# Optimization experiments

Hardware: AMD Instinct MI355X
Metric: run time of the kernel (lower is better)

## Reference

```python
import jax, jax.numpy as jnp
import numpy as np

WS = 8          # window size
NUM_HEADS = 12


def setup_inputs() -> dict:
    key = jax.random.key(0)
    k1, k2, k3 = jax.random.split(key, 3)
    B, N, C = 16, 4096, 384
    x = jax.random.normal(k1, (B, N, C), dtype=jnp.float32)
    # torch Linear weights stored as [in, out] so forward is x @ W
    qkv_w = jax.random.normal(k2, (C, 3 * C), dtype=jnp.float32) * (C ** -0.5)
    proj_w = jax.random.normal(k3, (C, C), dtype=jnp.float32) * (C ** -0.5)
    proj_b = jnp.zeros((C,), dtype=jnp.float32)
    return {"x": x, "qkv_w": qkv_w, "proj_w": proj_w, "proj_b": proj_b}


def reference(x, qkv_w, proj_w, proj_b):
    B, N, C = x.shape
    H = W = int(np.sqrt(N))
    hg, wg = H // WS, W // WS
    G = hg * wg
    nh = NUM_HEADS
    hd = C // nh
    scale = hd ** -0.5

    # window partition: [B, N, C] -> [B, hg, wg, ws, ws, C]
    xw = x.reshape(B, hg, WS, wg, WS, C).transpose(0, 1, 3, 2, 4, 5)
    xw = xw.reshape(B, G, WS * WS, C)

    # qkv projection -> [3, B, G, nh, ws*ws, hd]
    qkv = (xw @ qkv_w).reshape(B, G, WS * WS, 3, nh, hd)
    qkv = qkv.transpose(3, 0, 1, 4, 2, 5)
    q, k, v = qkv[0], qkv[1], qkv[2]

    attn = jnp.einsum('bgnqd,bgnkd->bgnqk', q, k) * scale
    attn = jax.nn.softmax(attn, axis=-1)
    out = jnp.einsum('bgnqk,bgnkd->bgnqd', attn, v)

    # merge heads and reverse window partition
    out = out.transpose(0, 1, 3, 2, 4).reshape(B, hg, wg, WS, WS, C)
    out = out.transpose(0, 1, 3, 2, 4, 5).reshape(B, N, C)

    return out @ proj_w + proj_b
```

## Files before the change

kernel.cpp:

```cpp
#include <hip/hip_runtime.h>
#include <stdint.h>

typedef unsigned short ushort_t;
typedef __bf16 bf16x8 __attribute__((ext_vector_type(8)));
typedef float floatx4 __attribute__((ext_vector_type(4)));
typedef float floatx16 __attribute__((ext_vector_type(16)));
typedef unsigned short ushort8 __attribute__((ext_vector_type(8)));

__device__ __forceinline__ ushort_t f2b(float f) {
  union { float f; unsigned u; } v; v.f = f;
  unsigned r = v.u + 0x7fffu + ((v.u >> 16) & 1u);
  return (ushort_t)(r >> 16);
}
__device__ __forceinline__ ushort_t b2u(float f) {
  union { __bf16 b; ushort_t u; } v; v.b = (__bf16)f; return v.u;
}
__device__ __forceinline__ bf16x8 cvt8(const float* p) {
  floatx4 f0 = *(const floatx4*)p;
  floatx4 f1 = *(const floatx4*)(p + 4);
  union { bf16x8 v; __bf16 e[8]; } u;
#pragma unroll
  for (int j = 0; j < 4; ++j) u.e[j] = (__bf16)f0[j];
#pragma unroll
  for (int j = 0; j < 4; ++j) u.e[4 + j] = (__bf16)f1[j];
  return u.v;
}

__device__ __forceinline__ unsigned cvtpk(float a, float b) {
  unsigned r;
  asm("v_cvt_pk_bf16_f32 %0, %1, %2" : "=v"(r) : "v"(a), "v"(b));
  return r;
}
__device__ __forceinline__ void plswap(unsigned& x, unsigned& y) {
  asm("v_permlane32_swap_b32 %0, %1" : "+v"(x), "+v"(y));
}

__device__ __forceinline__ void async16(const ushort_t* g, ushort_t* l) {
  __builtin_amdgcn_global_load_lds(
      (const __attribute__((address_space(1))) void*)g,
      (__attribute__((address_space(3))) void*)l, 16, 0, 0);
}

__global__ __launch_bounds__(256) void cvt_x(const float* __restrict__ src,
                                             ushort_t* __restrict__ dst, int n8) {
  int i = blockIdx.x * 256 + threadIdx.x;
  if (i < n8) *(bf16x8*)&dst[(size_t)i * 8] = cvt8(src + (size_t)i * 8);
}

__global__ void transpose_k(const float* __restrict__ src,
                            ushort_t* __restrict__ dst, int R, int Cc) {
  int idx = blockIdx.x * 256 + threadIdx.x;
  if (idx < R * Cc) {
    int r = idx / Cc, c = idx % Cc;
    dst[(size_t)c * R + r] = f2b(src[idx]);
  }
}

template <int C_F32>
__global__ __launch_bounds__(256) void gemm_bt(
    const ushort_t* __restrict__ A, int lda,
    const ushort_t* __restrict__ Bt,
    const float* __restrict__ bias, void* __restrict__ C_,
    int M, int N, int K) {
  __shared__ __align__(16) ushort_t As[128 * 64];
  __shared__ __align__(16) ushort_t Bs[128 * 64];
  const int t = threadIdx.x;
  const int nwg = gridDim.x;
  const int per = nwg >> 3;
  const int swz = (blockIdx.x & 7) * per + (blockIdx.x >> 3);
  const int ntn = N >> 7;
  const int m0 = (swz / ntn) << 7;
  const int n0 = (swz % ntn) << 7;
  const int w = t >> 6, lane = t & 63;
  const int wy = (w >> 1) << 6;
  const int wx = (w & 1) << 6;
  const int l15 = lane & 15;
  const int quad = lane >> 4;
  const int quad4 = quad << 2;
  floatx4 acc[4][4] = {};
  const int srow = t >> 3;
  const int sc = (((t & 7) ^ (srow & 7)) << 3);
  const ushort_t* gA = A + (size_t)(m0 + srow) * lda + sc;
  const ushort_t* gB = Bt + (size_t)(n0 + srow) * K + sc;
  for (int k0 = 0; k0 < K; k0 += 64) {
    __syncthreads();
#pragma unroll
    for (int r4 = 0; r4 < 4; ++r4) {
      async16(gA + (size_t)r4 * 32 * lda + k0, &As[r4 * 2048 + t * 8]);
      async16(gB + (size_t)r4 * 32 * K + k0, &Bs[r4 * 2048 + t * 8]);
    }
    __syncthreads();
#pragma unroll
    for (int kk = 0; kk < 2; ++kk) {
      bf16x8 af[4], bfr[4];
#pragma unroll
      for (int i = 0; i < 4; ++i) {
        int row = wy + i * 16 + l15;
        af[i] = *(const bf16x8*)&As[row * 64 + ((((kk << 2) | quad) ^ (row & 7)) << 3)];
      }
#pragma unroll
      for (int j = 0; j < 4; ++j) {
        int row = wx + j * 16 + l15;
        bfr[j] = *(const bf16x8*)&Bs[row * 64 + ((((kk << 2) | quad) ^ (row & 7)) << 3)];
      }
#pragma unroll
      for (int i = 0; i < 4; ++i)
#pragma unroll
        for (int j = 0; j < 4; ++j)
          acc[i][j] = __builtin_amdgcn_mfma_f32_16x16x32_bf16(
              af[i], bfr[j], acc[i][j], 0, 0, 0);
    }
  }
  float bv[4] = {0.f, 0.f, 0.f, 0.f};
  if (bias != nullptr) {
#pragma unroll
    for (int j = 0; j < 4; ++j) bv[j] = bias[n0 + wx + j * 16 + l15];
  }
#pragma unroll
  for (int i = 0; i < 4; ++i) {
#pragma unroll
    for (int r = 0; r < 4; ++r) {
      size_t row = (size_t)(m0 + wy + i * 16 + quad4 + r);
      if (C_F32) {
        float* cp = (float*)C_ + row * N + (n0 + wx + l15);
#pragma unroll
        for (int j = 0; j < 4; ++j) cp[j * 16] = acc[i][j][r] + bv[j];
      } else {
        ushort_t* cp = (ushort_t*)C_ + row * N + (n0 + wx + l15);
#pragma unroll
        for (int j = 0; j < 4; ++j) cp[j * 16] = f2b(acc[i][j][r] + bv[j]);
      }
    }
  }
}

__global__ __launch_bounds__(256, 2) void attn_proj(
    const ushort_t* __restrict__ QKV, const ushort_t* __restrict__ Bt,
    const float* __restrict__ bias, float* __restrict__ out) {
  __shared__ __align__(16) ushort_t Vt[4][32 * 72];
  __shared__ __align__(16) ushort_t Ao[64 * 384];
  const int blk = blockIdx.x;
  const int b = blk >> 6, g = blk & 63;
  const int gy = g >> 3, gx = g & 7;
  const int t = threadIdx.x, w = t >> 6, lane = t & 63;
  const int l31 = lane & 31, bh = lane >> 5;
  const int l15 = lane & 15, quad = lane >> 4, quad4 = quad << 2;
  const size_t bbase = (size_t)b * 4096 + (size_t)(gy * 8) * 64 + gx * 8;
  const float scale = 0.17677669529663687f;

  for (int hi = 0; hi < 3; ++hi) {
    const int h = w * 3 + hi;
    const size_t hq = (size_t)h * 32;

    {
      size_t row = bbase + (size_t)(lane >> 3) * 64 + (lane & 7);
      const ushort_t* vp = QKV + row * 1152 + 768 + hq;
#pragma unroll
      for (int i = 0; i < 4; ++i) {
        ushort8 vv = *(const ushort8*)(vp + i * 8);
#pragma unroll
        for (int j = 0; j < 8; ++j) Vt[w][(i * 8 + j) * 72 + lane] = vv[j];
      }
    }

    bf16x8 qf[2][2];
#pragma unroll
    for (int qt = 0; qt < 2; ++qt) {
      int tok = qt * 32 + l31;
      size_t row = bbase + (size_t)(tok >> 3) * 64 + (tok & 7);
#pragma unroll
      for (int dc = 0; dc < 2; ++dc)
        qf[qt][dc] = *(const bf16x8*)(QKV + row * 1152 + hq + dc * 16 + bh * 8);
    }

    floatx16 st[2][2] = {};
#pragma unroll
    for (int kt = 0; kt < 2; ++kt) {
      bf16x8 kf[2];
      int tok = kt * 32 + l31;
      size_t row = bbase + (size_t)(tok >> 3) * 64 + (tok & 7);
#pragma unroll
      for (int dc = 0; dc < 2; ++dc)
        kf[dc] = *(const bf16x8*)(QKV + row * 1152 + 384 + hq + dc * 16 + bh * 8);
#pragma unroll
      for (int qt = 0; qt < 2; ++qt)
#pragma unroll
        for (int dc = 0; dc < 2; ++dc)
          st[kt][qt] = __builtin_amdgcn_mfma_f32_32x32x16_bf16(
              kf[dc], qf[qt][dc], st[kt][qt], 0, 0, 0);
    }

    float rs[2] = {0.f, 0.f};
#pragma unroll
    for (int kt = 0; kt < 2; ++kt)
#pragma unroll
      for (int qt = 0; qt < 2; ++qt)
#pragma unroll
        for (int r = 0; r < 16; ++r) {
          float e = __expf(st[kt][qt][r] * scale);
          st[kt][qt][r] = e;
          rs[qt] += e;
        }
#pragma unroll
    for (int qt = 0; qt < 2; ++qt) rs[qt] += __shfl_xor(rs[qt], 32);
    float inv[2] = {1.0f / rs[0], 1.0f / rs[1]};

    floatx16 o[2] = {};
#pragma unroll
    for (int s = 0; s < 4; ++s) {
      const int kt = s >> 1, r1x = (s & 1) << 1;
      bf16x8 vf = *(const bf16x8*)&Vt[w][l31 * 72 + s * 16 + bh * 8];
#pragma unroll
      for (int qt = 0; qt < 2; ++qt) {
        float iv = inv[qt];
        unsigned x0 = cvtpk(st[kt][qt][4 * r1x + 0] * iv, st[kt][qt][4 * r1x + 1] * iv);
        unsigned x1 = cvtpk(st[kt][qt][4 * r1x + 2] * iv, st[kt][qt][4 * r1x + 3] * iv);
        unsigned y0 = cvtpk(st[kt][qt][4 * r1x + 4] * iv, st[kt][qt][4 * r1x + 5] * iv);
        unsigned y1 = cvtpk(st[kt][qt][4 * r1x + 6] * iv, st[kt][qt][4 * r1x + 7] * iv);
        plswap(x0, y0);
        plswap(x1, y1);
        union { unsigned d[4]; bf16x8 v; } pa;
        pa.d[0] = x0; pa.d[1] = x1; pa.d[2] = y0; pa.d[3] = y1;
        o[qt] = __builtin_amdgcn_mfma_f32_32x32x16_bf16(pa.v, vf, o[qt], 0, 0, 0);
      }
    }

    const int base64 = (h >> 1) << 6;
    const int cbase = ((h & 1) << 2) | (l31 >> 3);
    const int e7 = l31 & 7;
#pragma unroll
    for (int qt = 0; qt < 2; ++qt)
#pragma unroll
      for (int r = 0; r < 16; ++r) {
        int tok = qt * 32 + (r & 3) + 8 * (r >> 2) + 4 * bh;
        int c = cbase ^ (tok & 7);
        Ao[tok * 384 + base64 + (c << 3) + e7] = b2u(o[qt][r]);
      }
  }

  __syncthreads();

  floatx4 acc[4][6] = {};
  for (int ks = 0; ks < 12; ++ks) {
    bf16x8 af[4];
#pragma unroll
    for (int i = 0; i < 4; ++i) {
      int row = i * 16 + l15;
      int c = (((ks & 1) << 2) | quad) ^ (row & 7);
      af[i] = *(const bf16x8*)&Ao[row * 384 + ((ks >> 1) << 6) + (c << 3)];
    }
    bf16x8 bfr[6];
#pragma unroll
    for (int j = 0; j < 6; ++j) {
      int n = w * 96 + j * 16 + l15;
      bfr[j] = *(const bf16x8*)&Bt[(size_t)n * 384 + ks * 32 + (quad << 3)];
    }
#pragma unroll
    for (int i = 0; i < 4; ++i)
#pragma unroll
      for (int j = 0; j < 6; ++j)
        acc[i][j] = __builtin_amdgcn_mfma_f32_16x16x32_bf16(
            af[i], bfr[j], acc[i][j], 0, 0, 0);
  }

  float bv[6];
#pragma unroll
  for (int j = 0; j < 6; ++j) bv[j] = bias[w * 96 + j * 16 + l15];
#pragma unroll
  for (int i = 0; i < 4; ++i) {
#pragma unroll
    for (int r = 0; r < 4; ++r) {
      int tok = i * 16 + quad4 + r;
      size_t grow = bbase + (size_t)(tok >> 3) * 64 + (tok & 7);
      float* cp = out + grow * 384 + w * 96 + l15;
#pragma unroll
      for (int j = 0; j < 6; ++j) cp[j * 16] = acc[i][j][r] + bv[j];
    }
  }
}

extern "C" void kernel_launch(void* const* d_in, const int* in_sizes, int n_in,
                              void* d_out, int out_size, void* d_ws, size_t ws_size,
                              hipStream_t stream) {
  const float* x      = (const float*)d_in[0];
  const float* qkv_w  = (const float*)d_in[1];
  const float* proj_w = (const float*)d_in[2];
  const float* proj_b = (const float*)d_in[3];
  float* out = (float*)d_out;

  const int M = 16 * 4096;
  const size_t need =
      ((size_t)M * 1152 + (size_t)M * 384 + 1152 * 384 + 384 * 384) * 2;
  if (ws_size < need) return;

  ushort_t* qkv    = (ushort_t*)d_ws;
  ushort_t* xb     = qkv + (size_t)M * 1152;
  ushort_t* qkvwT  = xb + (size_t)M * 384;
  ushort_t* projwT = qkvwT + (size_t)1152 * 384;

  cvt_x<<<(M * 384 / 8 + 255) / 256, 256, 0, stream>>>(x, xb, M * 384 / 8);
  transpose_k<<<(384 * 1152 + 255) / 256, 256, 0, stream>>>(qkv_w, qkvwT, 384, 1152);
  transpose_k<<<(384 * 384 + 255) / 256, 256, 0, stream>>>(proj_w, projwT, 384, 384);

  gemm_bt<0><<<(M / 128) * (1152 / 128), 256, 0, stream>>>(
      xb, 384, qkvwT, nullptr, qkv, M, 1152, 384);

  attn_proj<<<16 * 64, 256, 0, stream>>>(qkv, projwT, proj_b, out);
}
```

Baseline: 329.6 us.

## Fuse fp32-to-bf16 input conversion into QKV GEMM and drop V LDS transpose

Removes the separate cvt_x kernel and bf16 copy of x; the QKV GEMM now reads fp32 x directly and converts it to bf16 while staging A tiles into LDS. In the attention kernel the V tile is no longer transposed through LDS but gathered with strided scalar global loads, K loads are hoisted ahead of the MFMAs, and occupancy is raised to 3 blocks per SM. This cuts one full read-write pass over x and LDS traffic, but the A loads become synchronous (no global_load_lds), each GEMM tile re-reads fp32 x nine times across N tiles, and the V gathers are uncoalesced 2-byte loads.

```diff
diff --git a/kernel.cpp b/kernel.cpp
--- a/kernel.cpp
+++ b/kernel.cpp
@@ -39,12 +39,6 @@
   __builtin_amdgcn_global_load_lds(
       (const __attribute__((address_space(1))) void*)g,
       (__attribute__((address_space(3))) void*)l, 16, 0, 0);
-}
-
-__global__ __launch_bounds__(256) void cvt_x(const float* __restrict__ src,
-                                             ushort_t* __restrict__ dst, int n8) {
-  int i = blockIdx.x * 256 + threadIdx.x;
-  if (i < n8) *(bf16x8*)&dst[(size_t)i * 8] = cvt8(src + (size_t)i * 8);
 }
 
 __global__ void transpose_k(const float* __restrict__ src,
@@ -56,12 +50,10 @@
   }
 }
 
-template <int C_F32>
-__global__ __launch_bounds__(256) void gemm_bt(
-    const ushort_t* __restrict__ A, int lda,
+__global__ __launch_bounds__(256) void gemm_qkv(
+    const float* __restrict__ A,
     const ushort_t* __restrict__ Bt,
-    const float* __restrict__ bias, void* __restrict__ C_,
-    int M, int N, int K) {
+    ushort_t* __restrict__ C, int M, int N, int K) {
   __shared__ __align__(16) ushort_t As[128 * 64];
   __shared__ __align__(16) ushort_t Bs[128 * 64];
   const int t = threadIdx.x;
@@ -80,14 +72,15 @@
   floatx4 acc[4][4] = {};
   const int srow = t >> 3;
   const int sc = (((t & 7) ^ (srow & 7)) << 3);
-  const ushort_t* gA = A + (size_t)(m0 + srow) * lda + sc;
+  const float* gA = A + (size_t)(m0 + srow) * K + sc;
   const ushort_t* gB = Bt + (size_t)(n0 + srow) * K + sc;
   for (int k0 = 0; k0 < K; k0 += 64) {
     __syncthreads();
 #pragma unroll
     for (int r4 = 0; r4 < 4; ++r4) {
-      async16(gA + (size_t)r4 * 32 * lda + k0, &As[r4 * 2048 + t * 8]);
       async16(gB + (size_t)r4 * 32 * K + k0, &Bs[r4 * 2048 + t * 8]);
+      bf16x8 av = cvt8(gA + (size_t)r4 * 32 * K + k0);
+      *(bf16x8*)&As[r4 * 2048 + t * 8] = av;
     }
     __syncthreads();
 #pragma unroll
@@ -111,33 +104,21 @@
               af[i], bfr[j], acc[i][j], 0, 0, 0);
     }
   }
-  float bv[4] = {0.f, 0.f, 0.f, 0.f};
-  if (bias != nullptr) {
-#pragma unroll
-    for (int j = 0; j < 4; ++j) bv[j] = bias[n0 + wx + j * 16 + l15];
-  }
 #pragma unroll
   for (int i = 0; i < 4; ++i) {
 #pragma unroll
     for (int r = 0; r < 4; ++r) {
       size_t row = (size_t)(m0 + wy + i * 16 + quad4 + r);
-      if (C_F32) {
-        float* cp = (float*)C_ + row * N + (n0 + wx + l15);
-#pragma unroll
-        for (int j = 0; j < 4; ++j) cp[j * 16] = acc[i][j][r] + bv[j];
-      } else {
-        ushort_t* cp = (ushort_t*)C_ + row * N + (n0 + wx + l15);
-#pragma unroll
-        for (int j = 0; j < 4; ++j) cp[j * 16] = f2b(acc[i][j][r] + bv[j]);
-      }
-    }
-  }
-}
-
-__global__ __launch_bounds__(256, 2) void attn_proj(
+      ushort_t* cp = C + row * N + (n0 + wx + l15);
+#pragma unroll
+      for (int j = 0; j < 4; ++j) cp[j * 16] = f2b(acc[i][j][r]);
+    }
+  }
+}
+
+__global__ __launch_bounds__(256, 3) void attn_proj(
     const ushort_t* __restrict__ QKV, const ushort_t* __restrict__ Bt,
     const float* __restrict__ bias, float* __restrict__ out) {
-  __shared__ __align__(16) ushort_t Vt[4][32 * 72];
   __shared__ __align__(16) ushort_t Ao[64 * 384];
   const int blk = blockIdx.x;
   const int b = blk >> 6, g = blk & 63;
@@ -152,17 +133,6 @@
     const int h = w * 3 + hi;
     const size_t hq = (size_t)h * 32;
 
-    {
-      size_t row = bbase + (size_t)(lane >> 3) * 64 + (lane & 7);
-      const ushort_t* vp = QKV + row * 1152 + 768 + hq;
-#pragma unroll
-      for (int i = 0; i < 4; ++i) {
-        ushort8 vv = *(const ushort8*)(vp + i * 8);
-#pragma unroll
-        for (int j = 0; j < 8; ++j) Vt[w][(i * 8 + j) * 72 + lane] = vv[j];
-      }
-    }
-
     bf16x8 qf[2][2];
 #pragma unroll
     for (int qt = 0; qt < 2; ++qt) {
@@ -172,23 +142,35 @@
       for (int dc = 0; dc < 2; ++dc)
         qf[qt][dc] = *(const bf16x8*)(QKV + row * 1152 + hq + dc * 16 + bh * 8);
     }
-
-    floatx16 st[2][2] = {};
+    bf16x8 kf[2][2];
 #pragma unroll
     for (int kt = 0; kt < 2; ++kt) {
-      bf16x8 kf[2];
       int tok = kt * 32 + l31;
       size_t row = bbase + (size_t)(tok >> 3) * 64 + (tok & 7);
 #pragma unroll
       for (int dc = 0; dc < 2; ++dc)
-        kf[dc] = *(const bf16x8*)(QKV + row * 1152 + 384 + hq + dc * 16 + bh * 8);
+        kf[kt][dc] = *(const bf16x8*)(QKV + row * 1152 + 384 + hq + dc * 16 + bh * 8);
+    }
+    bf16x8 vf[4];
+#pragma unroll
+    for (int s = 0; s < 4; ++s) {
+      const ushort_t* vbase =
+          QKV + (bbase + (size_t)(2 * s + bh) * 64) * 1152 + 768 + hq + l31;
+      union { ushort_t e[8]; bf16x8 v; } vu;
+#pragma unroll
+      for (int j = 0; j < 8; ++j) vu.e[j] = vbase[(size_t)j * 1152];
+      vf[s] = vu.v;
+    }
+
+    floatx16 st[2][2] = {};
+#pragma unroll
+    for (int kt = 0; kt < 2; ++kt)
 #pragma unroll
       for (int qt = 0; qt < 2; ++qt)
 #pragma unroll
         for (int dc = 0; dc < 2; ++dc)
           st[kt][qt] = __builtin_amdgcn_mfma_f32_32x32x16_bf16(
-              kf[dc], qf[qt][dc], st[kt][qt], 0, 0, 0);
-    }
+              kf[kt][dc], qf[qt][dc], st[kt][qt], 0, 0, 0);
 
     float rs[2] = {0.f, 0.f};
 #pragma unroll
@@ -209,7 +191,6 @@
 #pragma unroll
     for (int s = 0; s < 4; ++s) {
       const int kt = s >> 1, r1x = (s & 1) << 1;
-      bf16x8 vf = *(const bf16x8*)&Vt[w][l31 * 72 + s * 16 + bh * 8];
 #pragma unroll
       for (int qt = 0; qt < 2; ++qt) {
         float iv = inv[qt];
@@ -221,7 +202,7 @@
         plswap(x1, y1);
         union { unsigned d[4]; bf16x8 v; } pa;
         pa.d[0] = x0; pa.d[1] = x1; pa.d[2] = y0; pa.d[3] = y1;
-        o[qt] = __builtin_amdgcn_mfma_f32_32x32x16_bf16(pa.v, vf, o[qt], 0, 0, 0);
+        o[qt] = __builtin_amdgcn_mfma_f32_32x32x16_bf16(pa.v, vf[s], o[qt], 0, 0, 0);
       }
     }
 
@@ -290,20 +271,18 @@
 
   const int M = 16 * 4096;
   const size_t need =
-      ((size_t)M * 1152 + (size_t)M * 384 + 1152 * 384 + 384 * 384) * 2;
+      ((size_t)M * 1152 + 1152 * 384 + 384 * 384) * 2;
   if (ws_size < need) return;
 
   ushort_t* qkv    = (ushort_t*)d_ws;
-  ushort_t* xb     = qkv + (size_t)M * 1152;
-  ushort_t* qkvwT  = xb + (size_t)M * 384;
+  ushort_t* qkvwT  = qkv + (size_t)M * 1152;
   ushort_t* projwT = qkvwT + (size_t)1152 * 384;
 
-  cvt_x<<<(M * 384 / 8 + 255) / 256, 256, 0, stream>>>(x, xb, M * 384 / 8);
   transpose_k<<<(384 * 1152 + 255) / 256, 256, 0, stream>>>(qkv_w, qkvwT, 384, 1152);
   transpose_k<<<(384 * 384 + 255) / 256, 256, 0, stream>>>(proj_w, projwT, 384, 384);
 
-  gemm_bt<0><<<(M / 128) * (1152 / 128), 256, 0, stream>>>(
-      xb, 384, qkvwT, nullptr, qkv, M, 1152, 384);
+  gemm_qkv<<<(M / 128) * (1152 / 128), 256, 0, stream>>>(
+      x, qkvwT, qkv, M, 1152, 384);
 
   attn_proj<<<16 * 64, 256, 0, stream>>>(qkv, projwT, proj_b, out);
 }
```

Result: slower. 367.8 us (+11.6%).
